# Performance work log

Hardware: AMD Instinct MI355X
Metric: run time of the kernel (lower is better)

The kernel has to match this reference:

```python
import jax, jax.numpy as jnp
import numpy as np

EPS = 1e-08

def setup_inputs() -> dict:
    key = jax.random.key(0)
    k1, k2, k3, k4 = jax.random.split(key, 4)
    B, T, D, D_sample = 16, 512, 2048, 4096
    z_hist = jax.random.normal(k1, (B, T, D), dtype=jnp.float32)
    decay_rates = jax.random.normal(k2, (D_sample,), dtype=jnp.float32)
    idx_i = jax.random.randint(k3, (D_sample,), 0, D)
    idx_j = jax.random.randint(k4, (D_sample,), 0, D)
    return {"z_hist": z_hist, "decay_rates": decay_rates, "idx_i": idx_i, "idx_j": idx_j}

def reference(z_hist, decay_rates, idx_i, idx_j):
    B, T, D = z_hist.shape
    r = jax.nn.softplus(decay_rates)                      # [N]
    times = jnp.arange(T, dtype=z_hist.dtype)             # [T]
    # decay[t, n] = exp(-r_n * (T - 1 - t))
    decay = jnp.exp(-r[None, :] * (T - 1 - times)[:, None])  # [T, N]
    z_i = z_hist[:, :, idx_i]                              # [B, T, N]
    z_j = z_hist[:, :, idx_j]                              # [B, T, N]
    num = jnp.einsum('btn,btn,tn->bn', z_i, z_j, decay)    # [B, N]
    den = jnp.sqrt(decay.sum(axis=0) + EPS)                # [N]
    return num / den[None, :]
```

## Files before the change

kernel.cpp:

```cpp
#include <hip/hip_runtime.h>
#include <math.h>

#define B_    16
#define T_    512
#define D_    2048
#define DS_   4096
#define TG_   128
#define RS_   2052
#define EPS_  1e-8f
#define CLOG  16.0f


__device__ __forceinline__ float softplus_f(float x) {
    return (x > 20.f) ? x : log1pf(expf(x));
}

__device__ __forceinline__ void glds16(const float* g, float* l) {
    __builtin_amdgcn_global_load_lds((const __attribute__((address_space(1))) void*)g,
                                     (__attribute__((address_space(3))) void*)l,
                                     16, 0, 0);
}

__global__ __launch_bounds__(256) void pre_kernel(const float* __restrict__ decay_rates,
                                                  float* __restrict__ inv_den) {
    int n = blockIdx.x * 256 + threadIdx.x;
    float r = softplus_f(decay_rates[n]);
    float S = expm1f(-r * (float)T_) / expm1f(-r);
    inv_den[n] = 1.0f / sqrtf(S + EPS_);
}

__global__ __launch_bounds__(1024) void sort_kernel(const float* __restrict__ decay_rates,
                                                    const int* __restrict__ idx_i,
                                                    const int* __restrict__ idx_j,
                                                    float* __restrict__ g_s,
                                                    float* __restrict__ nr_s,
                                                    int* __restrict__ pair_s,
                                                    int* __restrict__ nout_s,
                                                    int* __restrict__ hcap_s,
                                                    int* __restrict__ tgmin_g,
                                                    int* __restrict__ smax_g) {
    __shared__ int hist[64];
    __shared__ int tgl[16];
    const int tid = threadIdx.x;
    if (tid < 64) hist[tid] = 0;
    __syncthreads();
    #pragma unroll
    for (int k = 0; k < 4; ++k) {
        int n = tid + k * 1024;
        float r = softplus_f(decay_rates[n]);
        float hf = CLOG / r;
        int h = (hf >= 511.f) ? 511 : (int)hf;
        atomicAdd(&hist[h >> 3], 1);
    }
    __syncthreads();
    if (tid == 0) {
        int run = 0;
        for (int q = 63; q >= 0; --q) { int c = hist[q]; hist[q] = run; run += c; }
    }
    __syncthreads();
    #pragma unroll
    for (int k = 0; k < 4; ++k) {
        int n = tid + k * 1024;
        float r = softplus_f(decay_rates[n]);
        float hf = CLOG / r;
        int h = (hf >= 511.f) ? 511 : (int)hf;
        int q = h >> 3;
        int pos = atomicAdd(&hist[q], 1);
        g_s[pos]    = expf(r);
        nr_s[pos]   = -r;
        pair_s[pos] = idx_i[n] | (idx_j[n] << 16);
        nout_s[pos] = n;
        hcap_s[pos] = (q << 3) | 7;
    }
    __syncthreads();
    if (tid < 16) {
        int h = hcap_s[tid * 256];
        int tm = (511 - h) >> 2;
        if (tm < 0) tm = 0;
        tgl[tid] = tm;
        tgmin_g[tid] = tm;
    }
    __syncthreads();
    if (tid < TG_) {
        int c = 0;
        #pragma unroll
        for (int s = 0; s < 16; ++s) c += (tgl[s] <= tid) ? 1 : 0;
        smax_g[tid] = c;
    }
}

__global__ __launch_bounds__(256) void main_kernel(const float* __restrict__ z,
                                                   const float* __restrict__ g_s,
                                                   const float* __restrict__ nr_s,
                                                   const int* __restrict__ pair_s,
                                                   const int* __restrict__ smax_g,
                                                   float* __restrict__ num) {
    __shared__ float rows[4 * RS_];
    const int tg   = blockIdx.x;
    const int b    = blockIdx.y;
    const int tid  = threadIdx.x;
    const int wave = tid >> 6, lane = tid & 63;
    const int tb   = tg * 4;
    const int smax = smax_g[tg];
    if (smax == 0) return;

    const float* src = z + ((size_t)b * T_ + tb + wave) * D_ + lane * 4;
    float* dst = rows + wave * RS_;
    #pragma unroll
    for (int s = 0; s < 8; ++s)
        glds16(src + s * 256, dst + s * 256);

    const float kb0 = (float)(511 - tb);
    int pair[16]; float g[16], w0[16];
    #pragma unroll
    for (int s = 0; s < 16; ++s) {
        if (s < smax) {
            int m = tid + s * 256;
            pair[s] = pair_s[m];
            g[s]    = g_s[m];
            w0[s]   = __expf(nr_s[m] * kb0);
        }
    }

    asm volatile("s_waitcnt vmcnt(0)" ::: "memory");
    __syncthreads();

    #pragma unroll
    for (int s = 0; s < 16; ++s) {
        if (s < smax) {
            int ci = pair[s] & 0xFFFF, cj = pair[s] >> 16;
            float vi0 = rows[ci],           vj0 = rows[cj];
            float vi1 = rows[RS_ + ci],     vj1 = rows[RS_ + cj];
            float vi2 = rows[2 * RS_ + ci], vj2 = rows[2 * RS_ + cj];
            float vi3 = rows[3 * RS_ + ci], vj3 = rows[3 * RS_ + cj];
            float gs = g[s];
            float h3 = vi3 * vj3;
            float h2 = fmaf(h3, gs, vi2 * vj2);
            float h1 = fmaf(h2, gs, vi1 * vj1);
            float h0 = fmaf(h1, gs, vi0 * vj0);
            num[((size_t)tg * B_ + b) * DS_ + tid + s * 256] = w0[s] * h0;
        }
    }
}

__global__ __launch_bounds__(256) void fin_kernel(const float* __restrict__ num,
                                                  const float* __restrict__ inv_den,
                                                  const int* __restrict__ nout_s,
                                                  const int* __restrict__ tgmin_g,
                                                  float* __restrict__ out) {
    int gt = blockIdx.x * 256 + threadIdx.x;
    int m  = gt & (DS_ - 1);
    int b  = gt >> 12;
    int tgmin = tgmin_g[m >> 8];
    float sum = 0.f;
    for (int tg = tgmin; tg < TG_; ++tg)
        sum += num[((size_t)tg * B_ + b) * DS_ + m];
    int n = nout_s[m];
    out[b * DS_ + n] = sum * inv_den[n];
}

extern "C" void kernel_launch(void* const* d_in, const int* in_sizes, int n_in,
                              void* d_out, int out_size, void* d_ws, size_t ws_size,
                              hipStream_t stream) {
    const float* z  = (const float*)d_in[0];
    const float* dr = (const float*)d_in[1];
    const int*   ii = (const int*)d_in[2];
    const int*   jj = (const int*)d_in[3];
    float* out = (float*)d_out;

    float* num     = (float*)d_ws;
    float* inv_den = num + (size_t)TG_ * B_ * DS_;
    float* g_s     = inv_den + DS_;
    float* nr_s    = g_s + DS_;
    int*   pair_s  = (int*)(nr_s + DS_);
    int*   nout_s  = pair_s + DS_;
    int*   hcap_s  = nout_s + DS_;
    int*   tgmin_g = hcap_s + DS_;
    int*   smax_g  = tgmin_g + 16;

    hipLaunchKernelGGL(pre_kernel, dim3(DS_ / 256), dim3(256), 0, stream, dr, inv_den);
    hipLaunchKernelGGL(sort_kernel, dim3(1), dim3(1024), 0, stream,
                       dr, ii, jj, g_s, nr_s, pair_s, nout_s, hcap_s, tgmin_g, smax_g);
    hipLaunchKernelGGL(main_kernel, dim3(TG_, B_), dim3(256), 0, stream,
                       z, g_s, nr_s, pair_s, smax_g, num);
    hipLaunchKernelGGL(fin_kernel, dim3((B_ * DS_) / 256), dim3(256), 0, stream,
                       num, inv_den, nout_s, tgmin_g, out);
}
```

Before: 146.9 us.

## Merge pre and sort kernels, gather parameters via permutation in main kernel

Folds the separate denominator kernel into the single-block sort kernel, removing one launch. The sort now writes only the permutation, and the main kernel gathers decay, pair indices and rates through that permutation instead of reading presorted arrays. It also moves the early-exit smax read after the async row loads are issued, and unrolls the reduction loop in the final kernel. In exchange the main kernel does an extra level of indirect global loads.

```diff
diff --git a/kernel.cpp b/kernel.cpp
--- a/kernel.cpp
+++ b/kernel.cpp
@@ -21,64 +21,53 @@
                                      16, 0, 0);
 }
 
-__global__ __launch_bounds__(256) void pre_kernel(const float* __restrict__ decay_rates,
-                                                  float* __restrict__ inv_den) {
-    int n = blockIdx.x * 256 + threadIdx.x;
-    float r = softplus_f(decay_rates[n]);
-    float S = expm1f(-r * (float)T_) / expm1f(-r);
-    inv_den[n] = 1.0f / sqrtf(S + EPS_);
-}
-
-__global__ __launch_bounds__(1024) void sort_kernel(const float* __restrict__ decay_rates,
-                                                    const int* __restrict__ idx_i,
-                                                    const int* __restrict__ idx_j,
-                                                    float* __restrict__ g_s,
-                                                    float* __restrict__ nr_s,
-                                                    int* __restrict__ pair_s,
+__global__ __launch_bounds__(1024) void prep_kernel(const float* __restrict__ decay_rates,
+                                                    float* __restrict__ inv_den,
+                                                    float* __restrict__ g_u,
+                                                    float* __restrict__ nr_u,
                                                     int* __restrict__ nout_s,
-                                                    int* __restrict__ hcap_s,
                                                     int* __restrict__ tgmin_g,
                                                     int* __restrict__ smax_g) {
     __shared__ int hist[64];
+    __shared__ int start_s[64];
     __shared__ int tgl[16];
     const int tid = threadIdx.x;
     if (tid < 64) hist[tid] = 0;
     __syncthreads();
+    float rv[4]; int qv[4];
     #pragma unroll
     for (int k = 0; k < 4; ++k) {
         int n = tid + k * 1024;
         float r = softplus_f(decay_rates[n]);
+        rv[k] = r;
         float hf = CLOG / r;
         int h = (hf >= 511.f) ? 511 : (int)hf;
-        atomicAdd(&hist[h >> 3], 1);
+        qv[k] = h >> 3;
+        atomicAdd(&hist[qv[k]], 1);
+        float S = expm1f(-r * (float)T_) / expm1f(-r);
+        inv_den[n] = 1.0f / sqrtf(S + EPS_);
+        g_u[n]     = expf(r);
+        nr_u[n]    = -r;
     }
     __syncthreads();
     if (tid == 0) {
         int run = 0;
-        for (int q = 63; q >= 0; --q) { int c = hist[q]; hist[q] = run; run += c; }
+        for (int q = 63; q >= 0; --q) { start_s[q] = run; run += hist[q]; }
     }
     __syncthreads();
-    #pragma unroll
-    for (int k = 0; k < 4; ++k) {
-        int n = tid + k * 1024;
-        float r = softplus_f(decay_rates[n]);
-        float hf = CLOG / r;
-        int h = (hf >= 511.f) ? 511 : (int)hf;
-        int q = h >> 3;
-        int pos = atomicAdd(&hist[q], 1);
-        g_s[pos]    = expf(r);
-        nr_s[pos]   = -r;
-        pair_s[pos] = idx_i[n] | (idx_j[n] << 16);
-        nout_s[pos] = n;
-        hcap_s[pos] = (q << 3) | 7;
-    }
-    __syncthreads();
-    if (tid < 16) {
-        int h = hcap_s[tid * 256];
-        int tm = (511 - h) >> 2;
-        if (tm < 0) tm = 0;
-        tgl[tid] = tm;
-        tgmin_g[tid] = tm;
+    if (tid < 64) hist[tid] = start_s[tid];
+    if (tid >= 64 && tid < 80) {
+        int s = tid - 64;
+        int R = s * 256;
+        int qs = 0;
+        for (int q = 63; q >= 0; --q) {
+            int nxt = (q == 0) ? DS_ : start_s[q - 1];
+            if (start_s[q] <= R && R < nxt) { qs = q; break; }
+        }
+        int h = (qs << 3) | 7;
+        int tm = (511 - h) >> 2; if (tm < 0) tm = 0;
+        tgl[s] = tm;
+        tgmin_g[s] = tm;
     }
     __syncthreads();
     if (tid < TG_) {
@@ -87,12 +76,20 @@
         for (int s = 0; s < 16; ++s) c += (tgl[s] <= tid) ? 1 : 0;
         smax_g[tid] = c;
     }
+    #pragma unroll
+    for (int k = 0; k < 4; ++k) {
+        int n = tid + k * 1024;
+        int pos = atomicAdd(&hist[qv[k]], 1);
+        nout_s[pos] = n;
+    }
 }
 
 __global__ __launch_bounds__(256) void main_kernel(const float* __restrict__ z,
-                                                   const float* __restrict__ g_s,
-                                                   const float* __restrict__ nr_s,
-                                                   const int* __restrict__ pair_s,
+                                                   const float* __restrict__ g_u,
+                                                   const float* __restrict__ nr_u,
+                                                   const int* __restrict__ idx_i,
+                                                   const int* __restrict__ idx_j,
+                                                   const int* __restrict__ nout_s,
                                                    const int* __restrict__ smax_g,
                                                    float* __restrict__ num) {
     __shared__ float rows[4 * RS_];
@@ -101,8 +98,6 @@
     const int tid  = threadIdx.x;
     const int wave = tid >> 6, lane = tid & 63;
     const int tb   = tg * 4;
-    const int smax = smax_g[tg];
-    if (smax == 0) return;
 
     const float* src = z + ((size_t)b * T_ + tb + wave) * D_ + lane * 4;
     float* dst = rows + wave * RS_;
@@ -110,15 +105,17 @@
     for (int s = 0; s < 8; ++s)
         glds16(src + s * 256, dst + s * 256);
 
+    const int smax = smax_g[tg];
     const float kb0 = (float)(511 - tb);
     int pair[16]; float g[16], w0[16];
     #pragma unroll
     for (int s = 0; s < 16; ++s) {
         if (s < smax) {
             int m = tid + s * 256;
-            pair[s] = pair_s[m];
-            g[s]    = g_s[m];
-            w0[s]   = __expf(nr_s[m] * kb0);
+            int n = nout_s[m];
+            pair[s] = idx_i[n] | (idx_j[n] << 16);
+            g[s]    = g_u[n];
+            w0[s]   = __expf(nr_u[n] * kb0);
         }
     }
 
@@ -153,6 +150,7 @@
     int b  = gt >> 12;
     int tgmin = tgmin_g[m >> 8];
     float sum = 0.f;
+    #pragma unroll 4
     for (int tg = tgmin; tg < TG_; ++tg)
         sum += num[((size_t)tg * B_ + b) * DS_ + m];
     int n = nout_s[m];
@@ -170,19 +168,16 @@
 
     float* num     = (float*)d_ws;
     float* inv_den = num + (size_t)TG_ * B_ * DS_;
-    float* g_s     = inv_den + DS_;
-    float* nr_s    = g_s + DS_;
-    int*   pair_s  = (int*)(nr_s + DS_);
-    int*   nout_s  = pair_s + DS_;
-    int*   hcap_s  = nout_s + DS_;
-    int*   tgmin_g = hcap_s + DS_;
+    float* g_u     = inv_den + DS_;
+    float* nr_u    = g_u + DS_;
+    int*   nout_s  = (int*)(nr_u + DS_);
+    int*   tgmin_g = nout_s + DS_;
     int*   smax_g  = tgmin_g + 16;
 
-    hipLaunchKernelGGL(pre_kernel, dim3(DS_ / 256), dim3(256), 0, stream, dr, inv_den);
-    hipLaunchKernelGGL(sort_kernel, dim3(1), dim3(1024), 0, stream,
-                       dr, ii, jj, g_s, nr_s, pair_s, nout_s, hcap_s, tgmin_g, smax_g);
+    hipLaunchKernelGGL(prep_kernel, dim3(1), dim3(1024), 0, stream,
+                       dr, inv_den, g_u, nr_u, nout_s, tgmin_g, smax_g);
     hipLaunchKernelGGL(main_kernel, dim3(TG_, B_), dim3(256), 0, stream,
-                       z, g_s, nr_s, pair_s, smax_g, num);
+                       z, g_u, nr_u, ii, jj, nout_s, smax_g, num);
     hipLaunchKernelGGL(fin_kernel, dim3((B_ * DS_) / 256), dim3(256), 0, stream,
                        num, inv_den, nout_s, tgmin_g, out);
 }
```

Result: faster. 135.2 us (-8.0%).
